# Performance work log

Measured on AMD Instinct MI355X. Metric: run time of the kernel, lower is better.

The kernel has to match this reference:

```python
import jax, jax.numpy as jnp
import numpy as np

N_NODES = 50000
N_EDGES = 800000
D = 128
H = 128


def setup_inputs() -> dict:
    key = jax.random.key(0)
    ks = jax.random.split(key, 8)
    s = 1.0 / np.sqrt(D)
    return {
        "x": jax.random.normal(ks[0], (N_NODES, D), dtype=jnp.float32),
        "edge_index": jax.random.randint(ks[1], (2, N_EDGES), 0, N_NODES, dtype=jnp.int64),
        "W1_l": jax.random.normal(ks[2], (D, H), dtype=jnp.float32) * s,
        "b1_l": jax.random.normal(ks[3], (H,), dtype=jnp.float32) * s,
        "W1_r": jax.random.normal(ks[4], (D, H), dtype=jnp.float32) * s,
        "W2_l": jax.random.normal(ks[5], (H, H), dtype=jnp.float32) * s,
        "b2_l": jax.random.normal(ks[6], (H,), dtype=jnp.float32) * s,
        "W2_r": jax.random.normal(ks[7], (H, H), dtype=jnp.float32) * s,
    }


def _sage_conv(x, src, dst, W_l, b_l, W_r, n_nodes):
    # mean aggregation of source features at destination nodes
    agg = jax.ops.segment_sum(x[src], dst, num_segments=n_nodes)          # [N, d]
    cnt = jax.ops.segment_sum(jnp.ones((src.shape[0],), x.dtype), dst,
                              num_segments=n_nodes)                        # [N]
    mean = agg / jnp.maximum(cnt, 1.0)[:, None]
    out = mean @ W_l + b_l + x @ W_r                                       # [N, h]
    # L2 normalize (normalize=True in SAGEConv)
    norm = jnp.linalg.norm(out, axis=-1, keepdims=True)
    return out / jnp.maximum(norm, 1e-12)


def reference(x, edge_index, W1_l, b1_l, W1_r, W2_l, b2_l, W2_r):
    src, dst = edge_index[0], edge_index[1]
    n = x.shape[0]
    h = jax.nn.relu(_sage_conv(x, src, dst, W1_l, b1_l, W1_r, n))
    h = jax.nn.relu(_sage_conv(h, src, dst, W2_l, b2_l, W2_r, n))
    return h
```

## Files before the change

kernel.cpp:

```cpp
#include <hip/hip_runtime.h>

#define N_NODES 50000
#define N_EDGES 800000
#define CAP 48

#define TILE   2048
#define NT     391
#define NT_PAD 392
#define NB     256
#define BIN_NODES 196

typedef __bf16 bf16_t;
typedef bf16_t bf16x8 __attribute__((ext_vector_type(8)));
typedef float f32x16 __attribute__((ext_vector_type(16)));

union Frag { float4 f4; bf16x8 h; };
union Pack8 { ushort u[8]; float4 f4; };

__device__ __forceinline__ ushort f2bf(float f) {
    unsigned u = __float_as_uint(f);
    return (ushort)((u + 0x7fffu + ((u >> 16) & 1u)) >> 16);
}
__device__ __forceinline__ float bf2f(unsigned bits) {
    return __uint_as_float(bits << 16);
}

__device__ __forceinline__ int detect_i64(const int* __restrict__ idx) {
    int lane = threadIdx.x & 63;
    int v = idx[2 * lane + 1];
    unsigned long long b = __ballot(v == 0);
    return (b == 0xFFFFFFFFFFFFFFFFull) ? 1 : 0;
}

__device__ __forceinline__ void load_edge(const int* __restrict__ idx, int f, int e,
                                          int& src, int& dst) {
    if (f) { src = idx[2 * e]; dst = idx[2 * N_EDGES + 2 * e]; }
    else   { src = idx[e];     dst = idx[N_EDGES + e]; }
}
__device__ __forceinline__ int load_dst(const int* __restrict__ idx, int f, int e) {
    return f ? idx[2 * N_EDGES + 2 * e] : idx[N_EDGES + e];
}

#define XBLK ((N_NODES * 64 + 255) / 256)
__global__ __launch_bounds__(256) void prep_hist_kernel(
        const float2* __restrict__ X, uint* __restrict__ Xb,
        const float* __restrict__ W1l, const float* __restrict__ W1r,
        const float* __restrict__ W2l, const float* __restrict__ W2r,
        ushort* __restrict__ Bp,
        const int* __restrict__ idx, uint* __restrict__ hist) {
    if (blockIdx.x < XBLK) {
        int i = blockIdx.x * 256 + threadIdx.x;
        if (i < N_NODES * 64) {
            float2 v = X[i];
            Xb[i] = ((uint)f2bf(v.y) << 16) | (uint)f2bf(v.x);
        }
        if (i < 8192) {
            int layer = i >> 12;
            int rec   = i & 4095;
            int t = rec >> 10;
            int s = (rec >> 6) & 15;
            int l = rec & 63;
            const float* Wl = layer ? W2l : W1l;
            const float* Wr = layer ? W2r : W1r;
            int n = t * 32 + (l & 31);
            int kb = s * 16 + (l >> 5) * 8;
            Pack8 o;
#pragma unroll
            for (int j = 0; j < 8; ++j) {
                int k = kb + j;
                float v = (k < 128) ? Wl[k * 128 + n] : Wr[(k - 128) * 128 + n];
                o.u[j] = f2bf(v);
            }
            *(float4*)(Bp + (size_t)i * 8) = o.f4;
        }
        return;
    }
    __shared__ uint h[NB];
    const int t   = blockIdx.x - XBLK;
    const int tid = threadIdx.x;
    h[tid] = 0;
    int f = detect_i64(idx);
    __syncthreads();
    const int e0 = t * TILE;
    const int e1 = min(e0 + TILE, N_EDGES);
    for (int e = e0 + tid; e < e1; e += 256) {
        int dst = load_dst(idx, f, e);
        atomicAdd(&h[(uint)dst / BIN_NODES], 1u);
    }
    __syncthreads();
    hist[(size_t)tid * NT_PAD + t] = h[tid];
}

__global__ __launch_bounds__(64) void scan_kernel(
        const uint* __restrict__ hist, uint* __restrict__ base,
        uint* __restrict__ total) {
    const int b = blockIdx.x;
    const int lane = threadIdx.x;
    uint run = 0;
    for (int c = 0; c < NT; c += 64) {
        int t = c + lane;
        uint v = (t < NT) ? hist[(size_t)b * NT_PAD + t] : 0u;
        uint x = v;
#pragma unroll
        for (int d = 1; d < 64; d <<= 1) {
            uint y = __shfl_up(x, d);
            if (lane >= d) x += y;
        }
        if (t < NT) base[(size_t)b * NT_PAD + t] = run + (x - v);
        run += __shfl(x, 63);
    }
    if (lane == 0) total[b] = run;
}

__global__ __launch_bounds__(256) void scatter_kernel(
        const int* __restrict__ idx, const uint* __restrict__ base,
        const uint* __restrict__ total, uint* __restrict__ eseg) {
    __shared__ uint s[NB];
    __shared__ uint binoff[NB];
    __shared__ uint lh[NB];
    const int t = blockIdx.x, tid = threadIdx.x;
    int f = detect_i64(idx);
    uint tot = total[tid];
    s[tid] = tot;
    __syncthreads();
#pragma unroll
    for (int d = 1; d < NB; d <<= 1) {
        uint v = (tid >= d) ? s[tid - d] : 0u;
        __syncthreads();
        s[tid] += v;
        __syncthreads();
    }
    binoff[tid] = (s[tid] - tot) + base[(size_t)tid * NT_PAD + t];
    lh[tid] = 0;
    __syncthreads();
    const int e0 = t * TILE;
    const int e1 = min(e0 + TILE, N_EDGES);
    for (int e = e0 + tid; e < e1; e += 256) {
        int src, dst;
        load_edge(idx, f, e, src, dst);
        uint b  = (uint)dst / BIN_NODES;
        uint dl = (uint)dst - b * BIN_NODES;
        uint r  = atomicAdd(&lh[b], 1u);
        eseg[binoff[b] + r] = (uint)src | (dl << 16);
    }
}

__global__ __launch_bounds__(256) void build_kernel(
        const uint* __restrict__ eseg, const uint* __restrict__ total,
        int* __restrict__ deg, ushort* __restrict__ esrc) {
    __shared__ uint s[NB];
    __shared__ uint cnt[BIN_NODES];
    __shared__ __align__(16) ushort lists[BIN_NODES * CAP];
    const int b = blockIdx.x, tid = threadIdx.x;
    uint tot = total[tid];
    s[tid] = tot;
    __syncthreads();
#pragma unroll
    for (int d = 1; d < NB; d <<= 1) {
        uint v = (tid >= d) ? s[tid - d] : 0u;
        __syncthreads();
        s[tid] += v;
        __syncthreads();
    }
    const uint start = (b == 0) ? 0u : s[b - 1];
    const uint cntb  = s[b] - start;
    for (int i = tid; i < BIN_NODES; i += 256) cnt[i] = 0;
    __syncthreads();
    for (uint i = tid; i < cntb; i += 256) {
        uint p  = eseg[start + i];
        uint dl = p >> 16;
        uint r  = atomicAdd(&cnt[dl], 1u);
        if (r < CAP) lists[dl * CAP + r] = (ushort)(p & 0xffffu);
    }
    __syncthreads();
    const int node0 = b * BIN_NODES;
    const int valid = min(BIN_NODES, N_NODES - node0);
    for (int i = tid; i < valid; i += 256)
        deg[node0 + i] = (int)cnt[i];
    const int nvec = valid * 6;
    uint4* dst4 = (uint4*)(esrc + (size_t)node0 * CAP);
    const uint4* src4 = (const uint4*)lists;
    for (int i = tid; i < nvec; i += 256) dst4[i] = src4[i];
}

__global__ __launch_bounds__(256) void gather_mean_kernel(
        const uint2* __restrict__ X2, const int* __restrict__ deg,
        const ushort* __restrict__ esrc, uint2* __restrict__ mean2) {
    const int wave = threadIdx.x >> 6;
    const int lane = threadIdx.x & 63;
    const int node = blockIdx.x * 8 + wave * 2 + (lane >> 5);
    const int l = lane & 31;
    if (node >= N_NODES) return;
    int dg = deg[node];
    if (dg > CAP) dg = CAP;
    const ushort* es = esrc + node * CAP;

    float c0[4] = {0, 0, 0, 0}, c1[4] = {0, 0, 0, 0};
    float c2[4] = {0, 0, 0, 0}, c3[4] = {0, 0, 0, 0};
    int p = 0;
    for (; p + 3 < dg; p += 4) {
        ushort4 ss = *(const ushort4*)(es + p);
        uint2 v0 = X2[(size_t)ss.x * 32 + l];
        uint2 v1 = X2[(size_t)ss.y * 32 + l];
        uint2 v2 = X2[(size_t)ss.z * 32 + l];
        uint2 v3 = X2[(size_t)ss.w * 32 + l];
        c0[0] += bf2f(v0.x & 0xffff); c0[1] += bf2f(v0.x >> 16);
        c0[2] += bf2f(v0.y & 0xffff); c0[3] += bf2f(v0.y >> 16);
        c1[0] += bf2f(v1.x & 0xffff); c1[1] += bf2f(v1.x >> 16);
        c1[2] += bf2f(v1.y & 0xffff); c1[3] += bf2f(v1.y >> 16);
        c2[0] += bf2f(v2.x & 0xffff); c2[1] += bf2f(v2.x >> 16);
        c2[2] += bf2f(v2.y & 0xffff); c2[3] += bf2f(v2.y >> 16);
        c3[0] += bf2f(v3.x & 0xffff); c3[1] += bf2f(v3.x >> 16);
        c3[2] += bf2f(v3.y & 0xffff); c3[3] += bf2f(v3.y >> 16);
    }
    for (; p < dg; ++p) {
        uint2 v = X2[(size_t)es[p] * 32 + l];
        c0[0] += bf2f(v.x & 0xffff); c0[1] += bf2f(v.x >> 16);
        c0[2] += bf2f(v.y & 0xffff); c0[3] += bf2f(v.y >> 16);
    }
    const float inv = 1.0f / (float)max(dg, 1);
    const float m0 = (c0[0] + c1[0] + c2[0] + c3[0]) * inv;
    const float m1 = (c0[1] + c1[1] + c2[1] + c3[1]) * inv;
    const float m2 = (c0[2] + c1[2] + c2[2] + c3[2]) * inv;
    const float m3 = (c0[3] + c1[3] + c2[3] + c3[3]) * inv;
    uint2 m;
    m.x = ((uint)f2bf(m1) << 16) | (uint)f2bf(m0);
    m.y = ((uint)f2bf(m3) << 16) | (uint)f2bf(m2);
    mean2[(size_t)node * 32 + l] = m;
}

template<bool OUT_F32>
__global__ __launch_bounds__(256) void gemm_mfma_kernel(
        const ushort* __restrict__ Amean, const ushort* Aself,
        const ushort* __restrict__ Bpack, const float* __restrict__ bias,
        void* Yout) {
    __shared__ float rs[2][64];
    const int tid = threadIdx.x;
    const int w = tid >> 6, l = tid & 63;
    const int lr = l & 31, lh = l >> 5;
    const int mrow0 = blockIdx.x * 64 + (w & 1) * 32;
    const int t0 = (w >> 1) * 2;

    f32x16 acc0, acc1;
#pragma unroll
    for (int i = 0; i < 16; ++i) { acc0[i] = 0.0f; acc1[i] = 0.0f; }

#pragma unroll
    for (int s = 0; s < 16; ++s) {
        const ushort* Ab = (s < 8) ? Amean : Aself;
        Frag a, b0, b1;
        a.f4  = *(const float4*)(Ab + (size_t)(mrow0 + lr) * 128 + (s & 7) * 16 + lh * 8);
        b0.f4 = *(const float4*)(Bpack + (size_t)(((t0) * 16 + s) * 64 + l) * 8);
        b1.f4 = *(const float4*)(Bpack + (size_t)(((t0 + 1) * 16 + s) * 64 + l) * 8);
        acc0 = __builtin_amdgcn_mfma_f32_32x32x16_bf16(a.h, b0.h, acc0, 0, 0, 0);
        acc1 = __builtin_amdgcn_mfma_f32_32x32x16_bf16(a.h, b1.h, acc1, 0, 0, 0);
    }

    const float bia0 = bias[t0 * 32 + lr];
    const float bia1 = bias[t0 * 32 + 32 + lr];
    float sq[16];
#pragma unroll
    for (int r = 0; r < 16; ++r) {
        float v0 = acc0[r] + bia0;
        float v1 = acc1[r] + bia1;
        acc0[r] = v0; acc1[r] = v1;
        float s_ = v0 * v0 + v1 * v1;
        s_ += __shfl_xor(s_, 1);
        s_ += __shfl_xor(s_, 2);
        s_ += __shfl_xor(s_, 4);
        s_ += __shfl_xor(s_, 8);
        s_ += __shfl_xor(s_, 16);
        sq[r] = s_;
    }
    if (lr == 0) {
#pragma unroll
        for (int r = 0; r < 16; ++r) {
            int rowl = (w & 1) * 32 + (r & 3) + 8 * (r >> 2) + 4 * lh;
            rs[w >> 1][rowl] = sq[r];
        }
    }
    __syncthreads();
#pragma unroll
    for (int r = 0; r < 16; ++r) {
        int rowl = (w & 1) * 32 + (r & 3) + 8 * (r >> 2) + 4 * lh;
        int grow = blockIdx.x * 64 + rowl;
        float tot = rs[0][rowl] + rs[1][rowl];
        float sc = 1.0f / fmaxf(sqrtf(tot), 1e-12f);
        if (grow < N_NODES) {
            float o0 = fmaxf(acc0[r] * sc, 0.0f);
            float o1 = fmaxf(acc1[r] * sc, 0.0f);
            if (OUT_F32) {
                float* Y = (float*)Yout;
                Y[(size_t)grow * 128 + t0 * 32 + lr]      = o0;
                Y[(size_t)grow * 128 + t0 * 32 + 32 + lr] = o1;
            } else {
                ushort* Y = (ushort*)Yout;
                Y[(size_t)grow * 128 + t0 * 32 + lr]      = f2bf(o0);
                Y[(size_t)grow * 128 + t0 * 32 + 32 + lr] = f2bf(o1);
            }
        }
    }
}

extern "C" void kernel_launch(void* const* d_in, const int* in_sizes, int n_in,
                              void* d_out, int out_size, void* d_ws, size_t ws_size,
                              hipStream_t stream) {
    const float* x    = (const float*)d_in[0];
    const int*   idx  = (const int*)d_in[1];
    const float* W1l  = (const float*)d_in[2];
    const float* b1l  = (const float*)d_in[3];
    const float* W1r  = (const float*)d_in[4];
    const float* W2l  = (const float*)d_in[5];
    const float* b2l  = (const float*)d_in[6];
    const float* W2r  = (const float*)d_in[7];
    float* out = (float*)d_out;

    int*    deg   = (int*)d_ws;
    ushort* esrc  = (ushort*)((int*)d_ws + 50016);
    uint*   hist  = (uint*)((int*)d_ws + 50016);
    uint*   base  = hist + NB * NT_PAD;
    uint*   meanb = (uint*)((int*)d_ws + 1250016);
    uint*   eseg  = meanb;
    uint*   total = meanb + 800000;
    uint*   xh    = (uint*)((int*)d_ws + 4450016);
    ushort* Bp    = (ushort*)((int*)d_ws + 7650016);

    prep_hist_kernel<<<XBLK + NT, 256, 0, stream>>>(
        (const float2*)x, xh, W1l, W1r, W2l, W2r, Bp, idx, hist);
    scan_kernel<<<NB, 64, 0, stream>>>(hist, base, total);
    scatter_kernel<<<NT, 256, 0, stream>>>(idx, base, total, eseg);
    build_kernel<<<NB, 256, 0, stream>>>(eseg, total, deg, esrc);

    const int gb = (N_NODES + 7) / 8;
    const int mb = (N_NODES + 63) / 64;

    gather_mean_kernel<<<gb, 256, 0, stream>>>(
        (const uint2*)xh, deg, esrc, (uint2*)meanb);
    gemm_mfma_kernel<false><<<mb, 256, 0, stream>>>(
        (const ushort*)meanb, (const ushort*)xh, Bp, b1l, (void*)xh);
    gather_mean_kernel<<<gb, 256, 0, stream>>>(
        (const uint2*)xh, deg, esrc, (uint2*)meanb);
    gemm_mfma_kernel<true><<<mb, 256, 0, stream>>>(
        (const ushort*)meanb, (const ushort*)xh, Bp + 4096 * 8, b2l, (void*)out);
}
```

Measured before the change: 220.2 us.

## Fuse neighbor mean gather into MFMA GEMM via swizzled shared memory

Merges the gather-mean kernel into the GEMM kernel. Each block computes the 64 neighbor means it needs into an XOR-swizzled LDS tile, then runs the MFMA loop reading the mean operand from LDS and the self operand from registers loaded up front. This removes the global write and re-read of the mean buffer and two kernel launches. Layer 1 now writes its output to a separate buffer (hbuf) instead of back into xh, which avoids a read/write race between blocks. In exchange, gather parallelism is fixed at 782 blocks with 16 KB of LDS each, so latency hiding in the gather phase may drop.

```diff
diff --git a/kernel.cpp b/kernel.cpp
--- a/kernel.cpp
+++ b/kernel.cpp
@@ -183,63 +183,72 @@
     for (int i = tid; i < nvec; i += 256) dst4[i] = src4[i];
 }
 
-__global__ __launch_bounds__(256) void gather_mean_kernel(
-        const uint2* __restrict__ X2, const int* __restrict__ deg,
-        const ushort* __restrict__ esrc, uint2* __restrict__ mean2) {
-    const int wave = threadIdx.x >> 6;
-    const int lane = threadIdx.x & 63;
-    const int node = blockIdx.x * 8 + wave * 2 + (lane >> 5);
-    const int l = lane & 31;
-    if (node >= N_NODES) return;
-    int dg = deg[node];
-    if (dg > CAP) dg = CAP;
-    const ushort* es = esrc + node * CAP;
-
-    float c0[4] = {0, 0, 0, 0}, c1[4] = {0, 0, 0, 0};
-    float c2[4] = {0, 0, 0, 0}, c3[4] = {0, 0, 0, 0};
-    int p = 0;
-    for (; p + 3 < dg; p += 4) {
-        ushort4 ss = *(const ushort4*)(es + p);
-        uint2 v0 = X2[(size_t)ss.x * 32 + l];
-        uint2 v1 = X2[(size_t)ss.y * 32 + l];
-        uint2 v2 = X2[(size_t)ss.z * 32 + l];
-        uint2 v3 = X2[(size_t)ss.w * 32 + l];
-        c0[0] += bf2f(v0.x & 0xffff); c0[1] += bf2f(v0.x >> 16);
-        c0[2] += bf2f(v0.y & 0xffff); c0[3] += bf2f(v0.y >> 16);
-        c1[0] += bf2f(v1.x & 0xffff); c1[1] += bf2f(v1.x >> 16);
-        c1[2] += bf2f(v1.y & 0xffff); c1[3] += bf2f(v1.y >> 16);
-        c2[0] += bf2f(v2.x & 0xffff); c2[1] += bf2f(v2.x >> 16);
-        c2[2] += bf2f(v2.y & 0xffff); c2[3] += bf2f(v2.y >> 16);
-        c3[0] += bf2f(v3.x & 0xffff); c3[1] += bf2f(v3.x >> 16);
-        c3[2] += bf2f(v3.y & 0xffff); c3[3] += bf2f(v3.y >> 16);
-    }
-    for (; p < dg; ++p) {
-        uint2 v = X2[(size_t)es[p] * 32 + l];
-        c0[0] += bf2f(v.x & 0xffff); c0[1] += bf2f(v.x >> 16);
-        c0[2] += bf2f(v.y & 0xffff); c0[3] += bf2f(v.y >> 16);
-    }
-    const float inv = 1.0f / (float)max(dg, 1);
-    const float m0 = (c0[0] + c1[0] + c2[0] + c3[0]) * inv;
-    const float m1 = (c0[1] + c1[1] + c2[1] + c3[1]) * inv;
-    const float m2 = (c0[2] + c1[2] + c2[2] + c3[2]) * inv;
-    const float m3 = (c0[3] + c1[3] + c2[3] + c3[3]) * inv;
-    uint2 m;
-    m.x = ((uint)f2bf(m1) << 16) | (uint)f2bf(m0);
-    m.y = ((uint)f2bf(m3) << 16) | (uint)f2bf(m2);
-    mean2[(size_t)node * 32 + l] = m;
-}
-
 template<bool OUT_F32>
-__global__ __launch_bounds__(256) void gemm_mfma_kernel(
-        const ushort* __restrict__ Amean, const ushort* Aself,
+__global__ __launch_bounds__(256) void gemm_fused_kernel(
+        const uint2* __restrict__ X2,
+        const int* __restrict__ deg, const ushort* __restrict__ esrc,
         const ushort* __restrict__ Bpack, const float* __restrict__ bias,
         void* Yout) {
+    __shared__ __align__(16) unsigned char Am[64 * 256];
     __shared__ float rs[2][64];
     const int tid = threadIdx.x;
     const int w = tid >> 6, l = tid & 63;
     const int lr = l & 31, lh = l >> 5;
-    const int mrow0 = blockIdx.x * 64 + (w & 1) * 32;
+    const int nb0 = blockIdx.x * 64;
+    const int mrow0 = nb0 + (w & 1) * 32;
     const int t0 = (w >> 1) * 2;
+    const ushort* Xus = (const ushort*)X2;
+
+    Frag selfA[8];
+#pragma unroll
+    for (int s2 = 0; s2 < 8; ++s2)
+        selfA[s2].f4 = *(const float4*)(Xus + (size_t)(mrow0 + lr) * 128 + s2 * 16 + lh * 8);
+
+    const int hw = tid >> 5;
+    const int gl = tid & 31;
+    for (int it = 0; it < 8; ++it) {
+        const int ln = it * 8 + hw;
+        const int node = nb0 + ln;
+        uint2 m; m.x = 0u; m.y = 0u;
+        if (node < N_NODES) {
+            int dg = deg[node];
+            if (dg > CAP) dg = CAP;
+            const ushort* es = esrc + node * CAP;
+            float c0[4] = {0, 0, 0, 0}, c1[4] = {0, 0, 0, 0};
+            float c2[4] = {0, 0, 0, 0}, c3[4] = {0, 0, 0, 0};
+            int p = 0;
+            for (; p + 3 < dg; p += 4) {
+                ushort4 ss = *(const ushort4*)(es + p);
+                uint2 v0 = X2[(size_t)ss.x * 32 + gl];
+                uint2 v1 = X2[(size_t)ss.y * 32 + gl];
+                uint2 v2 = X2[(size_t)ss.z * 32 + gl];
+                uint2 v3 = X2[(size_t)ss.w * 32 + gl];
+                c0[0] += bf2f(v0.x & 0xffff); c0[1] += bf2f(v0.x >> 16);
+                c0[2] += bf2f(v0.y & 0xffff); c0[3] += bf2f(v0.y >> 16);
+                c1[0] += bf2f(v1.x & 0xffff); c1[1] += bf2f(v1.x >> 16);
+                c1[2] += bf2f(v1.y & 0xffff); c1[3] += bf2f(v1.y >> 16);
+                c2[0] += bf2f(v2.x & 0xffff); c2[1] += bf2f(v2.x >> 16);
+                c2[2] += bf2f(v2.y & 0xffff); c2[3] += bf2f(v2.y >> 16);
+                c3[0] += bf2f(v3.x & 0xffff); c3[1] += bf2f(v3.x >> 16);
+                c3[2] += bf2f(v3.y & 0xffff); c3[3] += bf2f(v3.y >> 16);
+            }
+            for (; p < dg; ++p) {
+                uint2 v = X2[(size_t)es[p] * 32 + gl];
+                c0[0] += bf2f(v.x & 0xffff); c0[1] += bf2f(v.x >> 16);
+                c0[2] += bf2f(v.y & 0xffff); c0[3] += bf2f(v.y >> 16);
+            }
+            const float inv = 1.0f / (float)max(dg, 1);
+            const float m0 = (c0[0] + c1[0] + c2[0] + c3[0]) * inv;
+            const float m1 = (c0[1] + c1[1] + c2[1] + c3[1]) * inv;
+            const float m2 = (c0[2] + c1[2] + c2[2] + c3[2]) * inv;
+            const float m3 = (c0[3] + c1[3] + c2[3] + c3[3]) * inv;
+            m.x = ((uint)f2bf(m1) << 16) | (uint)f2bf(m0);
+            m.y = ((uint)f2bf(m3) << 16) | (uint)f2bf(m2);
+        }
+        const int slot = (gl >> 1) ^ (ln & 15);
+        *(uint2*)(&Am[ln * 256 + (slot << 4) + (gl & 1) * 8]) = m;
+    }
+    __syncthreads();
 
     f32x16 acc0, acc1;
 #pragma unroll
@@ -247,9 +256,14 @@
 
 #pragma unroll
     for (int s = 0; s < 16; ++s) {
-        const ushort* Ab = (s < 8) ? Amean : Aself;
         Frag a, b0, b1;
-        a.f4  = *(const float4*)(Ab + (size_t)(mrow0 + lr) * 128 + (s & 7) * 16 + lh * 8);
+        if (s < 8) {
+            const int rl = (w & 1) * 32 + lr;
+            const int slot = (s * 2 + lh) ^ (rl & 15);
+            a.f4 = *(const float4*)(&Am[rl * 256 + (slot << 4)]);
+        } else {
+            a = selfA[s - 8];
+        }
         b0.f4 = *(const float4*)(Bpack + (size_t)(((t0) * 16 + s) * 64 + l) * 8);
         b1.f4 = *(const float4*)(Bpack + (size_t)(((t0 + 1) * 16 + s) * 64 + l) * 8);
         acc0 = __builtin_amdgcn_mfma_f32_32x32x16_bf16(a.h, b0.h, acc0, 0, 0, 0);
@@ -319,9 +333,9 @@
     ushort* esrc  = (ushort*)((int*)d_ws + 50016);
     uint*   hist  = (uint*)((int*)d_ws + 50016);
     uint*   base  = hist + NB * NT_PAD;
-    uint*   meanb = (uint*)((int*)d_ws + 1250016);
-    uint*   eseg  = meanb;
-    uint*   total = meanb + 800000;
+    uint*   hbuf  = (uint*)((int*)d_ws + 1250016);
+    uint*   eseg  = hbuf;
+    uint*   total = hbuf + 800000;
     uint*   xh    = (uint*)((int*)d_ws + 4450016);
     ushort* Bp    = (ushort*)((int*)d_ws + 7650016);
 
@@ -331,15 +345,10 @@
     scatter_kernel<<<NT, 256, 0, stream>>>(idx, base, total, eseg);
     build_kernel<<<NB, 256, 0, stream>>>(eseg, total, deg, esrc);
 
-    const int gb = (N_NODES + 7) / 8;
     const int mb = (N_NODES + 63) / 64;
 
-    gather_mean_kernel<<<gb, 256, 0, stream>>>(
-        (const uint2*)xh, deg, esrc, (uint2*)meanb);
-    gemm_mfma_kernel<false><<<mb, 256, 0, stream>>>(
-        (const ushort*)meanb, (const ushort*)xh, Bp, b1l, (void*)xh);
-    gather_mean_kernel<<<gb, 256, 0, stream>>>(
-        (const uint2*)xh, deg, esrc, (uint2*)meanb);
-    gemm_mfma_kernel<true><<<mb, 256, 0, stream>>>(
-        (const ushort*)meanb, (const ushort*)xh, Bp + 4096 * 8, b2l, (void*)out);
-}
+    gemm_fused_kernel<false><<<mb, 256, 0, stream>>>(
+        (const uint2*)xh, deg, esrc, Bp, b1l, (void*)hbuf);
+    gemm_fused_kernel<true><<<mb, 256, 0, stream>>>(
+        (const uint2*)hbuf, deg, esrc, Bp + 4096 * 8, b2l, (void*)out);
+}
```

Result: slower. 231.4 us (+5.1%).
